# Performance work log

Hardware: AMD Instinct MI355X
Metric: run time of the kernel (lower is better)

## Reference

```python
import jax, jax.numpy as jnp
import numpy as np

C = 128          # hidden channels
N = 40000        # nodes
E = 640000       # edges (avg degree 16)
G = 64           # graphs in batch
STEPS = (5, 4, 3, 2, 1)  # num_layers of each GatedGraphConv


def setup_inputs() -> dict:
    key = jax.random.key(0)
    ks = jax.random.split(key, 9)
    x = jax.random.normal(ks[0], (N, C), jnp.float32)
    edge_index = jax.random.randint(ks[1], (2, E), 0, N, dtype=jnp.int64)
    edge_weights = jax.random.uniform(ks[2], (E,), jnp.float32)
    batch = jnp.sort(jax.random.randint(ks[3], (N,), 0, G, dtype=jnp.int64))
    s = 1.0 / np.sqrt(C)
    # conv_w[k, i] = per-step propagation weight of conv k (unused steps padded)
    conv_w = jax.random.uniform(ks[4], (5, 5, C, C), jnp.float32, -s, s)
    gru_wih = jax.random.uniform(ks[5], (5, 3 * C, C), jnp.float32, -s, s)
    gru_whh = jax.random.uniform(ks[6], (5, 3 * C, C), jnp.float32, -s, s)
    gru_bih = jax.random.uniform(ks[7], (5, 3 * C), jnp.float32, -s, s)
    gru_bhh = jax.random.uniform(ks[8], (5, 3 * C), jnp.float32, -s, s)
    gn_w = jnp.ones((4, C), jnp.float32)
    gn_b = jnp.zeros((4, C), jnp.float32)
    gn_ms = jnp.ones((4, C), jnp.float32)  # GraphNorm mean_scale
    return {"x": x, "edge_weights": edge_weights, "conv_w": conv_w,
            "gru_wih": gru_wih, "gru_whh": gru_whh, "gru_bih": gru_bih,
            "gru_bhh": gru_bhh, "gn_w": gn_w, "gn_b": gn_b, "gn_ms": gn_ms,
            "edge_index": edge_index, "batch": batch}


def _gru(m, h, wih, whh, bih, bhh):
    gi = m @ wih.T + bih
    gh = h @ whh.T + bhh
    ir, iz, inew = jnp.split(gi, 3, axis=-1)
    hr, hz, hn = jnp.split(gh, 3, axis=-1)
    r = jax.nn.sigmoid(ir + hr)
    z = jax.nn.sigmoid(iz + hz)
    n = jnp.tanh(inew + r * hn)
    return (1.0 - z) * n + z * h


def _ggc(x, W, wih, whh, bih, bhh, src, dst, ew, steps):
    # PyG GatedGraphConv: m = x W_i; aggregate sum of ew * m[src] at dst; GRU update.
    for i in range(steps):
        m = x @ W[i]
        msg = m[src]
        if ew is not None:
            msg = msg * ew[:, None]
        agg = jax.ops.segment_sum(msg, dst, num_segments=x.shape[0])
        x = _gru(agg, x, wih, whh, bih, bhh)
    return x


def _graph_norm(x, w, b, ms, eps=1e-5):
    # called with batch=None -> normalize over all nodes as one graph
    mean = jnp.mean(x, axis=0)
    xc = x - ms * mean
    var = jnp.mean(xc * xc, axis=0)
    return w * xc / jnp.sqrt(var + eps) + b


def reference(x, edge_weights, conv_w, gru_wih, gru_whh, gru_bih, gru_bhh,
              gn_w, gn_b, gn_ms, edge_index, batch):
    src, dst = edge_index[0], edge_index[1]
    lrelu = jax.nn.leaky_relu
    o = _ggc(x, conv_w[0], gru_wih[0], gru_whh[0], gru_bih[0], gru_bhh[0], src, dst, edge_weights, STEPS[0])
    o = _graph_norm(o, gn_w[0], gn_b[0], gn_ms[0])
    o = lrelu(o)
    o = _ggc(o, conv_w[1], gru_wih[1], gru_whh[1], gru_bih[1], gru_bhh[1], src, dst, edge_weights, STEPS[1])
    o = lrelu(o)
    o = _graph_norm(o, gn_w[1], gn_b[1], gn_ms[1])
    o = _ggc(o, conv_w[2], gru_wih[2], gru_whh[2], gru_bih[2], gru_bhh[2], src, dst, edge_weights, STEPS[2])
    o = lrelu(o)
    o = _graph_norm(o, gn_w[2], gn_b[2], gn_ms[2])
    o = _ggc(o, conv_w[3], gru_wih[3], gru_whh[3], gru_bih[3], gru_bhh[3], src, dst, edge_weights, STEPS[3])
    o = lrelu(o)
    o = _graph_norm(o, gn_w[3], gn_b[3], gn_ms[3])
    o = _ggc(o, conv_w[4], gru_wih[4], gru_whh[4], gru_bih[4], gru_bhh[4], src, dst, None, STEPS[4])
    o = lrelu(o)
    return jax.ops.segment_sum(o, batch, num_segments=G)
```

## Files before the change

### kernel.cpp

```cpp
#include <hip/hip_runtime.h>
#include <hip/hip_bf16.h>

#define NN 40000
#define EE 640000
#define CCH 128
#define GG 64

typedef __attribute__((ext_vector_type(8))) short short8;
typedef __attribute__((ext_vector_type(4))) float f32x4;

__device__ __forceinline__ float lrelu01(float v){ return v > 0.f ? v : 0.01f*v; }
__device__ __forceinline__ float sigm(float v){ return 1.f/(1.f + __expf(-v)); }
__device__ __forceinline__ float tanh_f(float v){
  v = fminf(fmaxf(v, -15.f), 15.f);
  const float t = __expf(2.f*v);
  return (t - 1.f)/(t + 1.f);
}
__device__ __forceinline__ unsigned short f2bf(float f){
  union { float f; unsigned int u; } v; v.f = f;
  const unsigned int r = v.u + 0x7FFFu + ((v.u >> 16) & 1u);
  return (unsigned short)(r >> 16);
}
__device__ __forceinline__ float bf2f(unsigned short h){
  union { unsigned int u; float f; } v; v.u = ((unsigned int)h) << 16;
  return v.f;
}
__device__ __forceinline__ void split2v(const float4 a, const float4 b, short8& hi, short8& lo){
  const float v[8] = {a.x,a.y,a.z,a.w,b.x,b.y,b.z,b.w};
#pragma unroll
  for (int i=0;i<8;++i){
    const unsigned short h = f2bf(v[i]);
    hi[i] = (short)h;
    lo[i] = (short)f2bf(v[i] - bf2f(h));
  }
}
__device__ __forceinline__ float LDF(const void* p, int f32, size_t i){
  return f32 ? ((const float*)p)[i] : bf2f(((const unsigned short*)p)[i]);
}
__device__ __forceinline__ int LDI(const void* p, int i64, size_t i){
  return i64 ? (int)((const long long*)p)[i] : ((const int*)p)[i];
}

__global__ __launch_bounds__(256) void k_detect(const unsigned short* __restrict__ xh,
                                                const unsigned int* __restrict__ ei,
                                                int* __restrict__ flags){
  __shared__ int s1[256], s2[256];
  const int t = threadIdx.x;
  int c1 = 0, c2 = 0;
  for (int i=0;i<8;++i){
    const unsigned short w = xh[t*8 + i];
    const int e = (w >> 7) & 0xFF;
    if (e < 100 || e > 140) c1++;
    const unsigned int o = ei[(t*8 + i)*2 + 1];
    if (o) c2++;
  }
  s1[t]=c1; s2[t]=c2; __syncthreads();
  for (int off=128; off; off>>=1){ if (t<off){ s1[t]+=s1[t+off]; s2[t]+=s2[t+off]; } __syncthreads(); }
  if (t==0){
    flags[0] = (s1[0] > 64) ? 1 : 0;
    flags[1] = (s2[0] < 16) ? 1 : 0;
  }
}

__global__ __launch_bounds__(256) void k_hist(const void* __restrict__ eidx, const int* __restrict__ flags,
                                              int* __restrict__ deg){
  const int e = blockIdx.x*256 + threadIdx.x;
  if (e >= EE) return;
  atomicAdd(&deg[LDI(eidx, flags[1], (size_t)EE + e)], 1);
}

__global__ __launch_bounds__(256) void k_scan1(const int* __restrict__ deg, int* __restrict__ bsum){
  __shared__ int s[256];
  const int t = threadIdx.x;
  const int i = blockIdx.x*256 + t;
  s[t] = (i < NN) ? deg[i] : 0;
  __syncthreads();
  for (int off=128; off; off>>=1){ if (t<off) s[t]+=s[t+off]; __syncthreads(); }
  if (t==0) bsum[blockIdx.x] = s[0];
}

__global__ __launch_bounds__(256) void k_scan2(const int* __restrict__ bsum, int* __restrict__ boff,
                                               int* __restrict__ roff){
  __shared__ int s[256];
  const int t = threadIdx.x;
  const int v = (t < 157) ? bsum[t] : 0;
  s[t] = v; __syncthreads();
  for (int off=1; off<256; off<<=1){
    const int u = (t>=off) ? s[t-off] : 0;
    __syncthreads(); s[t] += u; __syncthreads();
  }
  if (t < 157) boff[t] = s[t] - v;
  if (t == 0) roff[NN] = EE;
}

__global__ __launch_bounds__(256) void k_scan3(const int* __restrict__ deg, const int* __restrict__ boff,
                                               int* __restrict__ roff, int* __restrict__ pos){
  __shared__ int s[256];
  const int t = threadIdx.x;
  const int i = blockIdx.x*256 + t;
  const int v = (i < NN) ? deg[i] : 0;
  s[t] = v; __syncthreads();
  for (int off=1; off<256; off<<=1){
    const int u = (t>=off) ? s[t-off] : 0;
    __syncthreads(); s[t] += u; __syncthreads();
  }
  if (i < NN){
    const int ex = boff[blockIdx.x] + s[t] - v;
    roff[i] = ex; pos[i] = ex;
  }
}

__global__ __launch_bounds__(256) void k_scatter(const void* __restrict__ eidx, const void* __restrict__ ew,
                                                 const int* __restrict__ flags,
                                                 int* __restrict__ pos, int* __restrict__ es, float* __restrict__ ewt){
  const int e = blockIdx.x*256 + threadIdx.x;
  if (e >= EE) return;
  const int i64 = flags[1];
  const int d = LDI(eidx, i64, (size_t)EE + e);
  const int p = atomicAdd(&pos[d], 1);
  es[p] = LDI(eidx, i64, e);
  ewt[p] = LDF(ew, flags[0], e);
}

__global__ __launch_bounds__(256) void k_x2f(const void* __restrict__ xin, const int* __restrict__ flags,
                                             float* __restrict__ xf,
                                             const void* __restrict__ batch, int* __restrict__ bat32){
  const int i = blockIdx.x*256 + threadIdx.x;
  if (i < NN*CCH) xf[i] = LDF(xin, flags[0], i);
  if (i < NN) bat32[i] = LDI(batch, flags[1], i);
}

__global__ __launch_bounds__(256) void k_wcvt_bf(const void* __restrict__ w, const int* __restrict__ flags,
                                                 unsigned short* __restrict__ o, const int n){
  const int i = blockIdx.x*256 + threadIdx.x;
  if (i < n) o[i] = f2bf(LDF(w, flags[0], i));
}

__global__ __launch_bounds__(256) void k_mkWc(const void* __restrict__ cw, const void* __restrict__ wih,
                                              const int* __restrict__ flags,
                                              unsigned short* __restrict__ wcH, unsigned short* __restrict__ wcL){
  __shared__ unsigned short sW[128*128];
  __shared__ unsigned short sI[32*136];
  const int tid = threadIdx.x;
  const int t = blockIdx.x / 12, tile = blockIdx.x % 12;
  int L=0, s=t;
  if (t>=14){L=4;s=t-14;} else if(t>=12){L=3;s=t-12;} else if(t>=9){L=2;s=t-9;} else if(t>=5){L=1;s=t-5;}
  const int f32 = flags[0];
  const size_t woff = (size_t)(L*5+s)*16384;
  const size_t ioff = (size_t)L*49152 + (size_t)tile*32*128;
  for (int u=tid; u<16384; u+=256) sW[u] = f2bf(LDF(cw, f32, woff + u));
  for (int u=tid; u<4096; u+=256){
    const int r = u>>7, jj = u&127;
    sI[r*136 + jj] = f2bf(LDF(wih, f32, ioff + r*128 + jj));
  }
  __syncthreads();
  const int cl = tid & 31;
  const int kb = (tid>>5)*16;
  for (int k=kb; k<kb+16; ++k){
    float acc = 0.f;
#pragma unroll 4
    for (int j8=0; j8<16; ++j8){
      const short8 a = *(const short8*)(sW + k*128 + j8*8);
      const short8 b = *(const short8*)(sI + cl*136 + j8*8);
#pragma unroll
      for (int q=0;q<8;++q) acc += bf2f((unsigned short)a[q]) * bf2f((unsigned short)b[q]);
    }
    const unsigned short h = f2bf(acc);
    const unsigned short l = f2bf(acc - bf2f(h));
    const size_t oidx = (size_t)t*49152 + (size_t)(tile*32 + cl)*128 + k;
    wcH[oidx] = h; wcL[oidx] = l;
  }
}

__global__ __launch_bounds__(256) void k_agg(const float* __restrict__ m, const int* __restrict__ roff,
                                             const int* __restrict__ es, const float* __restrict__ ewt,
                                             float* __restrict__ agg, const int useW){
  const int node = (blockIdx.x*256 + threadIdx.x) >> 6;
  if (node >= NN) return;
  const int lane = threadIdx.x & 63;
  const int h = lane >> 5, j = lane & 31;
  const int beg = roff[node], end = roff[node+1];
  float ax=0.f, ay=0.f, az=0.f, aw=0.f;
  int e = beg + h;
  for (; e + 14 < end; e += 16){
    int s_[8]; float w_[8]; float4 v_[8];
#pragma unroll
    for (int q=0;q<8;++q) s_[q] = es[e + q*2];
#pragma unroll
    for (int q=0;q<8;++q) w_[q] = useW ? ewt[e + q*2] : 1.f;
#pragma unroll
    for (int q=0;q<8;++q) v_[q] = *(const float4*)(m + (size_t)s_[q]*CCH + j*4);
#pragma unroll
    for (int p=0;p<4;++p){
      const float w0 = w_[p*2], w1 = w_[p*2+1];
      const float4 v0 = v_[p*2], v1 = v_[p*2+1];
      ax += w0*v0.x + w1*v1.x; ay += w0*v0.y + w1*v1.y;
      az += w0*v0.z + w1*v1.z; aw += w0*v0.w + w1*v1.w;
    }
  }
  for (; e + 2 < end; e += 4){
    const int s0 = es[e], s1 = es[e+2];
    const float w0 = useW ? ewt[e] : 1.f;
    const float w1 = useW ? ewt[e+2] : 1.f;
    const float4 v0 = *(const float4*)(m + (size_t)s0*CCH + j*4);
    const float4 v1 = *(const float4*)(m + (size_t)s1*CCH + j*4);
    ax += w0*v0.x + w1*v1.x; ay += w0*v0.y + w1*v1.y;
    az += w0*v0.z + w1*v1.z; aw += w0*v0.w + w1*v1.w;
  }
  if (e < end){
    const int s0 = es[e];
    const float w0 = useW ? ewt[e] : 1.f;
    const float4 v0 = *(const float4*)(m + (size_t)s0*CCH + j*4);
    ax += w0*v0.x; ay += w0*v0.y; az += w0*v0.z; aw += w0*v0.w;
  }
  ax += __shfl_xor(ax, 32); ay += __shfl_xor(ay, 32);
  az += __shfl_xor(az, 32); aw += __shfl_xor(aw, 32);
  if (h == 0){
    float4 ov; ov.x=ax; ov.y=ay; ov.z=az; ov.w=aw;
    *(float4*)(agg + (size_t)node*CCH + j*4) = ov;
  }
}

__global__ __launch_bounds__(512) void k_gru(const float* __restrict__ xg,
                                             float* __restrict__ xf,
                                             const unsigned short* __restrict__ wcH,
                                             const unsigned short* __restrict__ wcL,
                                             const unsigned short* __restrict__ whB,
                                             const void* __restrict__ bih, const void* __restrict__ bhh,
                                             const size_t boff, const int* __restrict__ flags){
  __shared__ unsigned short s_w[9*32*128];
  const int tid = threadIdx.x;
  const int wv = tid >> 6;
  const int lane = tid & 63;
  const int quad = lane >> 4;
  const int ln = lane & 15;
  const int m0 = blockIdx.x*128 + wv*16;
  const int f32 = flags[0];
  short8 fah[4], fal[4], fxh[4], fxl[4];
  {
    int arow = m0 + ln; if (arow >= NN) arow = NN-1;
    const float* pa = xg + (size_t)arow*CCH + quad*8;
    const float* px = xf + (size_t)arow*CCH + quad*8;
#pragma unroll
    for (int kk=0;kk<4;++kk){
      split2v(*(const float4*)(pa+kk*32), *(const float4*)(pa+kk*32+4), fah[kk], fal[kk]);
      split2v(*(const float4*)(px+kk*32), *(const float4*)(px+kk*32+4), fxh[kk], fxl[kk]);
    }
  }
#pragma unroll 1
  for (int ct=0; ct<4; ++ct){
    __syncthreads();
    for (int u = tid; u < 4608; u += 512){
      const int chunk = u >> 9;
      const int rem = u & 511;
      const int c = rem >> 4, p = rem & 15;
      const int mat = chunk / 3, g = chunk - mat*3;
      const unsigned short* msrc = (mat==0) ? wcH : ((mat==1) ? wcL : whB);
      const unsigned short* src = msrc + ((size_t)(g*CCH + ct*32 + c)*CCH + p*8);
      *(short8*)(s_w + chunk*4096 + c*128 + ((p ^ (c & 15))*8)) = *(const short8*)src;
    }
    __syncthreads();
#pragma unroll 1
    for (int hf=0; hf<2; ++hf){
      const int cl = hf*16 + ln;
      f32x4 acci[3], acch[3];
#pragma unroll
      for (int g=0;g<3;++g){ acci[g] = (f32x4){0.f,0.f,0.f,0.f}; acch[g] = (f32x4){0.f,0.f,0.f,0.f}; }
#pragma unroll
      for (int kk=0;kk<4;++kk){
        const int sw = ((kk*4+quad) ^ ln)*8;
#pragma unroll
        for (int g=0;g<3;++g){
          const short8 bh_ = *(const short8*)(s_w + g*4096     + cl*128 + sw);
          const short8 bl_ = *(const short8*)(s_w + (3+g)*4096 + cl*128 + sw);
          const short8 bb_ = *(const short8*)(s_w + (6+g)*4096 + cl*128 + sw);
          acci[g] = __builtin_amdgcn_mfma_f32_16x16x32_bf16(fah[kk], bh_, acci[g], 0, 0, 0);
          acci[g] = __builtin_amdgcn_mfma_f32_16x16x32_bf16(fal[kk], bh_, acci[g], 0, 0, 0);
          acci[g] = __builtin_amdgcn_mfma_f32_16x16x32_bf16(fah[kk], bl_, acci[g], 0, 0, 0);
          acch[g] = __builtin_amdgcn_mfma_f32_16x16x32_bf16(fxh[kk], bb_, acch[g], 0, 0, 0);
          acch[g] = __builtin_amdgcn_mfma_f32_16x16x32_bf16(fxl[kk], bb_, acch[g], 0, 0, 0);
        }
      }
      const int col = ct*32 + cl;
      float bi[3], bh[3];
#pragma unroll
      for (int g=0;g<3;++g){
        bi[g] = LDF(bih, f32, boff + g*CCH + col);
        bh[g] = LDF(bhh, f32, boff + g*CCH + col);
      }
#pragma unroll
      for (int r=0;r<4;++r){
        const int row = m0 + quad*4 + r;
        if (row < NN){
          const size_t idx = (size_t)row*CCH + col;
          const float h = xf[idx];
          const float rr = sigm(acci[0][r] + acch[0][r] + bi[0] + bh[0]);
          const float zz = sigm(acci[1][r] + acch[1][r] + bi[1] + bh[1]);
          const float nv = tanh_f(acci[2][r] + bi[2] + rr*(acch[2][r] + bh[2]));
          xf[idx] = (1.f - zz)*nv + zz*h;
        }
      }
    }
  }
}

__global__ __launch_bounds__(256) void k_gn_stats(const float* __restrict__ x, float* __restrict__ accum, const int pre){
  const int tid = threadIdx.x;
  const int ch = tid & 127;
  const int half = tid >> 7;
  const int node0 = blockIdx.x * 128;
  float s = 0.f, s2 = 0.f;
  for (int r = half; r < 128; r += 2){
    const int n = node0 + r;
    if (n >= NN) break;
    float v = x[(size_t)n*CCH + ch];
    if (pre) v = lrelu01(v);
    s += v; s2 += v*v;
  }
  __shared__ float buf[256];
  buf[tid] = s; __syncthreads();
  if (tid < 128) atomicAdd(&accum[ch], buf[tid] + buf[tid+128]);
  __syncthreads();
  buf[tid] = s2; __syncthreads();
  if (tid < 128) atomicAdd(&accum[128+ch], buf[tid] + buf[tid+128]);
}

__global__ __launch_bounds__(256) void k_gn_apply(float* __restrict__ xf, const float* __restrict__ accum,
                                                  const void* __restrict__ gw, const void* __restrict__ gb,
                                                  const void* __restrict__ gms, const size_t off,
                                                  const int* __restrict__ flags, const int mode){
  const int i = blockIdx.x*256 + threadIdx.x;
  const int ch = i & 127;
  const int f32 = flags[0];
  const float inv = 1.f/(float)NN;
  const float mean = accum[ch]*inv;
  const float m2 = accum[128+ch]*inv;
  const float ms = LDF(gms, f32, off + ch);
  const float var = m2 - 2.f*ms*mean*mean + ms*ms*mean*mean;
  const float sc = LDF(gw, f32, off + ch) / sqrtf(var + 1e-5f);
  const float sh = LDF(gb, f32, off + ch) - sc*ms*mean;
#pragma unroll
  for (int r=0;r<8;++r){
    const int idx = i + r*640000;
    float v = xf[idx];
    if (mode == 1) v = lrelu01(v);
    v = sc*v + sh;
    if (mode == 0) v = lrelu01(v);
    xf[idx] = v;
  }
}

__global__ __launch_bounds__(256) void k_final(const float* __restrict__ x, const int* __restrict__ bat,
                                               float* __restrict__ outf){
  const int t = threadIdx.x;
  const int ch = t & 127;
  const int half = t >> 7;
  const int n0 = blockIdx.x*32;
  int cur = -1; float acc = 0.f;
  for (int r = half; r < 32; r += 2){
    const int n = n0 + r;
    const int b = bat[n];
    if (b != cur){
      if (cur >= 0) atomicAdd(&outf[cur*CCH + ch], acc);
      cur = b; acc = 0.f;
    }
    acc += lrelu01(x[(size_t)n*CCH + ch]);
  }
  if (cur >= 0) atomicAdd(&outf[cur*CCH + ch], acc);
}

__global__ __launch_bounds__(256) void k_store(const float* __restrict__ outf, const int* __restrict__ flags, void* __restrict__ out){
  const int i = blockIdx.x*256 + threadIdx.x;
  if (i >= GG*CCH) return;
  if (flags[0]) ((float*)out)[i] = outf[i];
  else ((unsigned short*)out)[i] = f2bf(outf[i]);
}

extern "C" void kernel_launch(void* const* d_in, const int* in_sizes, int n_in,
                              void* d_out, int out_size, void* d_ws, size_t ws_size,
                              hipStream_t stream){
  const void* x_in = d_in[0];
  const void* ew   = d_in[1];
  const void* cw   = d_in[2];
  const void* wih  = d_in[3];
  const void* whh  = d_in[4];
  const void* bih  = d_in[5];
  const void* bhh  = d_in[6];
  const void* gnw  = d_in[7];
  const void* gnb  = d_in[8];
  const void* gnms = d_in[9];
  const void* eidx  = d_in[10];
  const void* batch = d_in[11];

  float* base = (float*)d_ws;
  size_t o = 0;
  float* xf     = base + o; o += (size_t)NN*CCH;
  float* xg     = base + o; o += (size_t)NN*CCH;
  unsigned short* wcH = (unsigned short*)(base + o); o += 15*384*CCH/2;
  unsigned short* wcL = (unsigned short*)(base + o); o += 15*384*CCH/2;
  unsigned short* whB5= (unsigned short*)(base + o); o += 5*384*CCH/2;
  float* ewt    = base + o; o += EE;
  int* flags    = (int*)(base + o); o += 2;
  int* bat32    = (int*)(base + o); o += NN;
  int* bsum     = (int*)(base + o); o += 160;
  int* boff2    = (int*)(base + o); o += 160;
  float* outf   = base + o; o += GG*CCH;
  float* gnacc  = base + o; o += 1024;
  int* deg      = (int*)(base + o); o += NN;
  int* roff     = (int*)(base + o); o += NN+1;
  int* pos      = (int*)(base + o); o += NN;
  int* es       = (int*)(base + o); o += EE;

  hipMemsetAsync(outf, 0, (size_t)(GG*CCH + 1024 + NN)*4, stream);

  k_detect<<<1,256,0,stream>>>((const unsigned short*)x_in, (const unsigned int*)eidx, flags);
  k_hist<<<2500,256,0,stream>>>(eidx, flags, deg);
  k_scan1<<<157,256,0,stream>>>(deg, bsum);
  k_scan2<<<1,256,0,stream>>>(bsum, boff2, roff);
  k_scan3<<<157,256,0,stream>>>(deg, boff2, roff, pos);
  k_scatter<<<2500,256,0,stream>>>(eidx, ew, flags, pos, es, ewt);
  k_x2f<<<20000,256,0,stream>>>(x_in, flags, xf, batch, bat32);
  k_wcvt_bf<<<960,256,0,stream>>>(whh, flags, whB5, 5*384*CCH);
  k_mkWc<<<180,256,0,stream>>>(cw, wih, flags, wcH, wcL);

  const int steps[5] = {5,4,3,2,1};
  int t = 0;
  for (int L=0; L<5; ++L){
    for (int s=0; s<steps[L]; ++s){
      k_agg<<<10000,256,0,stream>>>(xf, roff, es, ewt, xg, (L<4) ? 1 : 0);
      k_gru<<<313,512,0,stream>>>(xg, xf,
                                  wcH + (size_t)t*384*CCH, wcL + (size_t)t*384*CCH,
                                  whB5 + (size_t)L*384*CCH, bih, bhh, (size_t)L*384, flags);
      t++;
    }
    if (L < 4){
      const int pre = (L==0) ? 0 : 1;
      k_gn_stats<<<313,256,0,stream>>>(xf, gnacc + L*256, pre);
      k_gn_apply<<<2500,256,0,stream>>>(xf, gnacc + L*256, gnw, gnb, gnms, (size_t)L*CCH, flags, pre);
    }
  }
  k_final<<<1250,256,0,stream>>>(xf, bat32, outf);
  k_store<<<32,256,0,stream>>>(outf, flags, d_out);
}
```

Baseline: 1.720 ms.

## Fuse GraphNorm apply and leaky-ReLU into the next aggregation and GRU input loads

The separate full-tensor GraphNorm apply pass is replaced by a tiny kernel that computes per-channel scale and shift. The affine transform plus leaky-ReLU is then applied on the fly to gathered neighbor rows in the first aggregation, and to the hidden-state loads in the first GRU step of each layer. This removes a full read-modify-write of the node features. In exchange, each of about 16 gathered edges per node recomputes the transform. The GRU also caches its biases in shared memory and preloads its hidden-state values into registers, which raises register pressure.

```diff
diff --git a/kernel.cpp b/kernel.cpp
--- a/kernel.cpp
+++ b/kernel.cpp
@@ -24,6 +24,10 @@
 __device__ __forceinline__ float bf2f(unsigned short h){
   union { unsigned int u; float f; } v; v.u = ((unsigned int)h) << 16;
   return v.f;
+}
+__device__ __forceinline__ float Tx(float v, float sc, float sh, int tmode){
+  if (tmode == 0) return lrelu01(sc*v + sh);
+  return sc*lrelu01(v) + sh;
 }
 __device__ __forceinline__ void split2v(const float4 a, const float4 b, short8& hi, short8& lo){
   const float v[8] = {a.x,a.y,a.z,a.w,b.x,b.y,b.z,b.w};
@@ -174,7 +178,8 @@
 
 __global__ __launch_bounds__(256) void k_agg(const float* __restrict__ m, const int* __restrict__ roff,
                                              const int* __restrict__ es, const float* __restrict__ ewt,
-                                             float* __restrict__ agg, const int useW){
+                                             float* __restrict__ agg, const int useW,
+                                             const float* __restrict__ par, const int tmode){
   const int node = (blockIdx.x*256 + threadIdx.x) >> 6;
   if (node >= NN) return;
   const int lane = threadIdx.x & 63;
@@ -182,36 +187,83 @@
   const int beg = roff[node], end = roff[node+1];
   float ax=0.f, ay=0.f, az=0.f, aw=0.f;
   int e = beg + h;
-  for (; e + 14 < end; e += 16){
-    int s_[8]; float w_[8]; float4 v_[8];
-#pragma unroll
-    for (int q=0;q<8;++q) s_[q] = es[e + q*2];
-#pragma unroll
-    for (int q=0;q<8;++q) w_[q] = useW ? ewt[e + q*2] : 1.f;
-#pragma unroll
-    for (int q=0;q<8;++q) v_[q] = *(const float4*)(m + (size_t)s_[q]*CCH + j*4);
-#pragma unroll
-    for (int p=0;p<4;++p){
-      const float w0 = w_[p*2], w1 = w_[p*2+1];
-      const float4 v0 = v_[p*2], v1 = v_[p*2+1];
+  if (tmode < 0){
+    for (; e + 14 < end; e += 16){
+      int s_[8]; float w_[8]; float4 v_[8];
+#pragma unroll
+      for (int q=0;q<8;++q) s_[q] = es[e + q*2];
+#pragma unroll
+      for (int q=0;q<8;++q) w_[q] = useW ? ewt[e + q*2] : 1.f;
+#pragma unroll
+      for (int q=0;q<8;++q) v_[q] = *(const float4*)(m + (size_t)s_[q]*CCH + j*4);
+#pragma unroll
+      for (int p=0;p<4;++p){
+        const float w0 = w_[p*2], w1 = w_[p*2+1];
+        const float4 v0 = v_[p*2], v1 = v_[p*2+1];
+        ax += w0*v0.x + w1*v1.x; ay += w0*v0.y + w1*v1.y;
+        az += w0*v0.z + w1*v1.z; aw += w0*v0.w + w1*v1.w;
+      }
+    }
+    for (; e + 2 < end; e += 4){
+      const int s0 = es[e], s1 = es[e+2];
+      const float w0 = useW ? ewt[e] : 1.f;
+      const float w1 = useW ? ewt[e+2] : 1.f;
+      const float4 v0 = *(const float4*)(m + (size_t)s0*CCH + j*4);
+      const float4 v1 = *(const float4*)(m + (size_t)s1*CCH + j*4);
       ax += w0*v0.x + w1*v1.x; ay += w0*v0.y + w1*v1.y;
       az += w0*v0.z + w1*v1.z; aw += w0*v0.w + w1*v1.w;
     }
-  }
-  for (; e + 2 < end; e += 4){
-    const int s0 = es[e], s1 = es[e+2];
-    const float w0 = useW ? ewt[e] : 1.f;
-    const float w1 = useW ? ewt[e+2] : 1.f;
-    const float4 v0 = *(const float4*)(m + (size_t)s0*CCH + j*4);
-    const float4 v1 = *(const float4*)(m + (size_t)s1*CCH + j*4);
-    ax += w0*v0.x + w1*v1.x; ay += w0*v0.y + w1*v1.y;
-    az += w0*v0.z + w1*v1.z; aw += w0*v0.w + w1*v1.w;
-  }
-  if (e < end){
-    const int s0 = es[e];
-    const float w0 = useW ? ewt[e] : 1.f;
-    const float4 v0 = *(const float4*)(m + (size_t)s0*CCH + j*4);
-    ax += w0*v0.x; ay += w0*v0.y; az += w0*v0.z; aw += w0*v0.w;
+    if (e < end){
+      const int s0 = es[e];
+      const float w0 = useW ? ewt[e] : 1.f;
+      const float4 v0 = *(const float4*)(m + (size_t)s0*CCH + j*4);
+      ax += w0*v0.x; ay += w0*v0.y; az += w0*v0.z; aw += w0*v0.w;
+    }
+  } else {
+    const float4 sc4 = *(const float4*)(par + j*4);
+    const float4 sh4 = *(const float4*)(par + 128 + j*4);
+    for (; e + 14 < end; e += 16){
+      int s_[8]; float w_[8]; float4 v_[8];
+#pragma unroll
+      for (int q=0;q<8;++q) s_[q] = es[e + q*2];
+#pragma unroll
+      for (int q=0;q<8;++q) w_[q] = useW ? ewt[e + q*2] : 1.f;
+#pragma unroll
+      for (int q=0;q<8;++q){
+        float4 v = *(const float4*)(m + (size_t)s_[q]*CCH + j*4);
+        v.x = Tx(v.x, sc4.x, sh4.x, tmode); v.y = Tx(v.y, sc4.y, sh4.y, tmode);
+        v.z = Tx(v.z, sc4.z, sh4.z, tmode); v.w = Tx(v.w, sc4.w, sh4.w, tmode);
+        v_[q] = v;
+      }
+#pragma unroll
+      for (int p=0;p<4;++p){
+        const float w0 = w_[p*2], w1 = w_[p*2+1];
+        const float4 v0 = v_[p*2], v1 = v_[p*2+1];
+        ax += w0*v0.x + w1*v1.x; ay += w0*v0.y + w1*v1.y;
+        az += w0*v0.z + w1*v1.z; aw += w0*v0.w + w1*v1.w;
+      }
+    }
+    for (; e + 2 < end; e += 4){
+      const int s0 = es[e], s1 = es[e+2];
+      const float w0 = useW ? ewt[e] : 1.f;
+      const float w1 = useW ? ewt[e+2] : 1.f;
+      float4 v0 = *(const float4*)(m + (size_t)s0*CCH + j*4);
+      float4 v1 = *(const float4*)(m + (size_t)s1*CCH + j*4);
+      v0.x=Tx(v0.x,sc4.x,sh4.x,tmode); v0.y=Tx(v0.y,sc4.y,sh4.y,tmode);
+      v0.z=Tx(v0.z,sc4.z,sh4.z,tmode); v0.w=Tx(v0.w,sc4.w,sh4.w,tmode);
+      v1.x=Tx(v1.x,sc4.x,sh4.x,tmode); v1.y=Tx(v1.y,sc4.y,sh4.y,tmode);
+      v1.z=Tx(v1.z,sc4.z,sh4.z,tmode); v1.w=Tx(v1.w,sc4.w,sh4.w,tmode);
+      ax += w0*v0.x + w1*v1.x; ay += w0*v0.y + w1*v1.y;
+      az += w0*v0.z + w1*v1.z; aw += w0*v0.w + w1*v1.w;
+    }
+    if (e < end){
+      const int s0 = es[e];
+      const float w0 = useW ? ewt[e] : 1.f;
+      float4 v0 = *(const float4*)(m + (size_t)s0*CCH + j*4);
+      v0.x=Tx(v0.x,sc4.x,sh4.x,tmode); v0.y=Tx(v0.y,sc4.y,sh4.y,tmode);
+      v0.z=Tx(v0.z,sc4.z,sh4.z,tmode); v0.w=Tx(v0.w,sc4.w,sh4.w,tmode);
+      ax += w0*v0.x; ay += w0*v0.y; az += w0*v0.z; aw += w0*v0.w;
+    }
   }
   ax += __shfl_xor(ax, 32); ay += __shfl_xor(ay, 32);
   az += __shfl_xor(az, 32); aw += __shfl_xor(aw, 32);
@@ -227,8 +279,10 @@
                                              const unsigned short* __restrict__ wcL,
                                              const unsigned short* __restrict__ whB,
                                              const void* __restrict__ bih, const void* __restrict__ bhh,
-                                             const size_t boff, const int* __restrict__ flags){
+                                             const size_t boff, const int* __restrict__ flags,
+                                             const float* __restrict__ par, const int tmode){
   __shared__ unsigned short s_w[9*32*128];
+  __shared__ float s_bias[768];
   const int tid = threadIdx.x;
   const int wv = tid >> 6;
   const int lane = tid & 63;
@@ -236,7 +290,10 @@
   const int ln = lane & 15;
   const int m0 = blockIdx.x*128 + wv*16;
   const int f32 = flags[0];
+  for (int u = tid; u < 768; u += 512)
+    s_bias[u] = (u < 384) ? LDF(bih, f32, boff + u) : LDF(bhh, f32, boff + (u - 384));
   short8 fah[4], fal[4], fxh[4], fxl[4];
+  float hv[8][4];
   {
     int arow = m0 + ln; if (arow >= NN) arow = NN-1;
     const float* pa = xg + (size_t)arow*CCH + quad*8;
@@ -244,7 +301,33 @@
 #pragma unroll
     for (int kk=0;kk<4;++kk){
       split2v(*(const float4*)(pa+kk*32), *(const float4*)(pa+kk*32+4), fah[kk], fal[kk]);
-      split2v(*(const float4*)(px+kk*32), *(const float4*)(px+kk*32+4), fxh[kk], fxl[kk]);
+      float4 xa = *(const float4*)(px+kk*32);
+      float4 xb = *(const float4*)(px+kk*32+4);
+      if (tmode >= 0){
+        const int ch0 = quad*8 + kk*32;
+        const float4 sa = *(const float4*)(par + ch0);
+        const float4 sb = *(const float4*)(par + ch0 + 4);
+        const float4 ha = *(const float4*)(par + 128 + ch0);
+        const float4 hb = *(const float4*)(par + 128 + ch0 + 4);
+        xa.x=Tx(xa.x,sa.x,ha.x,tmode); xa.y=Tx(xa.y,sa.y,ha.y,tmode);
+        xa.z=Tx(xa.z,sa.z,ha.z,tmode); xa.w=Tx(xa.w,sa.w,ha.w,tmode);
+        xb.x=Tx(xb.x,sb.x,hb.x,tmode); xb.y=Tx(xb.y,sb.y,hb.y,tmode);
+        xb.z=Tx(xb.z,sb.z,hb.z,tmode); xb.w=Tx(xb.w,sb.w,hb.w,tmode);
+      }
+      split2v(xa, xb, fxh[kk], fxl[kk]);
+    }
+  }
+#pragma unroll
+  for (int ih=0; ih<8; ++ih){
+    const int col = ih*16 + ln;
+    float sc = 1.f, sh = 0.f;
+    if (tmode >= 0){ sc = par[col]; sh = par[128 + col]; }
+#pragma unroll
+    for (int r=0;r<4;++r){
+      int row = m0 + quad*4 + r; if (row >= NN) row = NN-1;
+      float v = xf[(size_t)row*CCH + col];
+      if (tmode >= 0) v = Tx(v, sc, sh, tmode);
+      hv[ih][r] = v;
     }
   }
 #pragma unroll 1
@@ -285,15 +368,16 @@
       float bi[3], bh[3];
 #pragma unroll
       for (int g=0;g<3;++g){
-        bi[g] = LDF(bih, f32, boff + g*CCH + col);
-        bh[g] = LDF(bhh, f32, boff + g*CCH + col);
-      }
+        bi[g] = s_bias[g*CCH + col];
+        bh[g] = s_bias[384 + g*CCH + col];
+      }
+      const int ih = ct*2 + hf;
 #pragma unroll
       for (int r=0;r<4;++r){
         const int row = m0 + quad*4 + r;
         if (row < NN){
           const size_t idx = (size_t)row*CCH + col;
-          const float h = xf[idx];
+          const float h = hv[ih][r];
           const float rr = sigm(acci[0][r] + acch[0][r] + bi[0] + bh[0]);
           const float zz = sigm(acci[1][r] + acch[1][r] + bi[1] + bh[1]);
           const float nv = tanh_f(acci[2][r] + bi[2] + rr*(acch[2][r] + bh[2]));
@@ -325,29 +409,19 @@
   if (tid < 128) atomicAdd(&accum[128+ch], buf[tid] + buf[tid+128]);
 }
 
-__global__ __launch_bounds__(256) void k_gn_apply(float* __restrict__ xf, const float* __restrict__ accum,
-                                                  const void* __restrict__ gw, const void* __restrict__ gb,
-                                                  const void* __restrict__ gms, const size_t off,
-                                                  const int* __restrict__ flags, const int mode){
-  const int i = blockIdx.x*256 + threadIdx.x;
-  const int ch = i & 127;
+__global__ void k_gn_final(const float* __restrict__ accum, const void* __restrict__ gw,
+                           const void* __restrict__ gb, const void* __restrict__ gms,
+                           const size_t off, const int* __restrict__ flags, float* __restrict__ par){
+  const int j = threadIdx.x;
   const int f32 = flags[0];
   const float inv = 1.f/(float)NN;
-  const float mean = accum[ch]*inv;
-  const float m2 = accum[128+ch]*inv;
-  const float ms = LDF(gms, f32, off + ch);
+  const float mean = accum[j]*inv;
+  const float m2 = accum[128+j]*inv;
+  const float ms = LDF(gms, f32, off + j);
   const float var = m2 - 2.f*ms*mean*mean + ms*ms*mean*mean;
-  const float sc = LDF(gw, f32, off + ch) / sqrtf(var + 1e-5f);
-  const float sh = LDF(gb, f32, off + ch) - sc*ms*mean;
-#pragma unroll
-  for (int r=0;r<8;++r){
-    const int idx = i + r*640000;
-    float v = xf[idx];
-    if (mode == 1) v = lrelu01(v);
-    v = sc*v + sh;
-    if (mode == 0) v = lrelu01(v);
-    xf[idx] = v;
-  }
+  const float sc = LDF(gw, f32, off + j) / sqrtf(var + 1e-5f);
+  par[j] = sc;
+  par[128+j] = LDF(gb, f32, off + j) - sc*ms*mean;
 }
 
 __global__ __launch_bounds__(256) void k_final(const float* __restrict__ x, const int* __restrict__ bat,
@@ -400,6 +474,7 @@
   unsigned short* wcL = (unsigned short*)(base + o); o += 15*384*CCH/2;
   unsigned short* whB5= (unsigned short*)(base + o); o += 5*384*CCH/2;
   float* ewt    = base + o; o += EE;
+  float* par    = base + o; o += 256;
   int* flags    = (int*)(base + o); o += 2;
   int* bat32    = (int*)(base + o); o += NN;
   int* bsum     = (int*)(base + o); o += 160;
@@ -425,18 +500,22 @@
 
   const int steps[5] = {5,4,3,2,1};
   int t = 0;
+  int tmode = -1;
   for (int L=0; L<5; ++L){
     for (int s=0; s<steps[L]; ++s){
-      k_agg<<<10000,256,0,stream>>>(xf, roff, es, ewt, xg, (L<4) ? 1 : 0);
+      k_agg<<<10000,256,0,stream>>>(xf, roff, es, ewt, xg, (L<4) ? 1 : 0, par, tmode);
       k_gru<<<313,512,0,stream>>>(xg, xf,
                                   wcH + (size_t)t*384*CCH, wcL + (size_t)t*384*CCH,
-                                  whB5 + (size_t)L*384*CCH, bih, bhh, (size_t)L*384, flags);
+                                  whB5 + (size_t)L*384*CCH, bih, bhh, (size_t)L*384, flags,
+                                  par, tmode);
+      tmode = -1;
       t++;
     }
     if (L < 4){
       const int pre = (L==0) ? 0 : 1;
       k_gn_stats<<<313,256,0,stream>>>(xf, gnacc + L*256, pre);
-      k_gn_apply<<<2500,256,0,stream>>>(xf, gnacc + L*256, gnw, gnb, gnms, (size_t)L*CCH, flags, pre);
+      k_gn_final<<<1,128,0,stream>>>(gnacc + L*256, gnw, gnb, gnms, (size_t)L*CCH, flags, par);
+      tmode = pre;
     }
   }
   k_final<<<1250,256,0,stream>>>(xf, bat32, outf);
```

After: 1.880 ms. 9.3% more time.
